# Performance work log

Hardware: AMD Instinct MI355X
Metric: run time of the kernel (lower is better)

The kernel has to match this reference:

```python
import jax, jax.numpy as jnp
import numpy as np

N, E, IN, H, OUT, CD = 50000, 800000, 64, 128, 128, 2


def _lin(key, fi, fo):
    # PyTorch nn.Linear default init: U(-1/sqrt(fan_in), 1/sqrt(fan_in))
    k1, k2 = jax.random.split(key)
    s = 1.0 / np.sqrt(fi)
    W = jax.random.uniform(k1, (fi, fo), minval=-s, maxval=s, dtype=jnp.float32)
    b = jax.random.uniform(k2, (fo,), minval=-s, maxval=s, dtype=jnp.float32)
    return W, b


def setup_inputs() -> dict:
    key = jax.random.key(0)
    ks = jax.random.split(key, 12)
    feat = jax.random.normal(ks[0], (N, IN), dtype=jnp.float32)
    offsets = jax.random.normal(ks[1], (E, CD), dtype=jnp.float32)
    src = jax.random.randint(ks[2], (E,), 0, N)
    dst = jax.random.randint(ks[3], (E,), 0, N)
    kW1, kb1 = _lin(ks[4], CD, H)
    kW2, kb2 = _lin(ks[5], H, IN)
    sW1, sb1 = _lin(ks[6], IN, H)
    sW2, sb2 = _lin(ks[7], H, H)
    mW1, mb1 = _lin(ks[8], IN + H, H)
    mW2, mb2 = _lin(ks[9], H, H)
    mW3, mb3 = _lin(ks[10], H, H)
    mW4, mb4 = _lin(ks[11], H, OUT)
    return dict(feat=feat, offsets=offsets, src=src, dst=dst,
                kW1=kW1, kb1=kb1, kW2=kW2, kb2=kb2,
                sW1=sW1, sb1=sb1, sW2=sW2, sb2=sb2,
                mW1=mW1, mb1=mb1, mW2=mW2, mb2=mb2,
                mW3=mW3, mb3=mb3, mW4=mW4, mb4=mb4)


def reference(feat, offsets, src, dst, kW1, kb1, kW2, kb2, sW1, sb1, sW2, sb2,
              mW1, mb1, mW2, mb2, mW3, mb3, mW4, mb4):
    elu = jax.nn.elu
    n = feat.shape[0]
    # per-edge kernel weights from offsets: [E, IN]
    kw = elu(offsets @ kW1 + kb1) @ kW2 + kb2
    # dist_fn == 'eculidean': score = 1 / (||offsets||_1 + 0.001), edge softmax per dst node
    score = 1.0 / (jnp.sum(jnp.abs(offsets), axis=1) + 0.001)  # [E]
    mx = jax.lax.stop_gradient(jax.ops.segment_max(score, dst, num_segments=n))
    ex = jnp.exp(score - mx[dst])
    w = ex / jax.ops.segment_sum(ex, dst, num_segments=n)[dst]  # [E]
    # u_mul_e + sum aggregation: gather src feats, scale by per-edge weights, scatter-add to dst
    m = feat[src] * (w[:, None] * kw)                     # [E, IN]
    agg = jax.ops.segment_sum(m, dst, num_segments=n)     # [N, IN]
    # self branch
    h_self = elu(feat @ sW1 + sb1) @ sW2 + sb2            # [N, H]
    # concat + MLP head
    h = jnp.concatenate([agg, h_self], axis=1)            # [N, IN+H]
    h = elu(h @ mW1 + mb1)
    h = elu(h @ mW2 + mb2)
    h = elu(h @ mW3 + mb3)
    return h @ mW4 + mb4                                  # [N, OUT]
```

## Files before the change

kernel.cpp:

```cpp
#include <hip/hip_runtime.h>
#include <hip/hip_bf16.h>
#include <math.h>

#define N_NODES 50000
#define N_EDGES 800000
#define NB_SCAN ((N_NODES + 255) / 256)

typedef _Float16 half8 __attribute__((ext_vector_type(8)));
typedef _Float16 half4 __attribute__((ext_vector_type(4)));
typedef float f32x4 __attribute__((ext_vector_type(4)));

__device__ __forceinline__ float elu_f(float x) { return x > 0.f ? x : __expf(x) - 1.f; }
__device__ __forceinline__ float edge_score(float2 o) {
    return 1.f / (fabsf(o.x) + fabsf(o.y) + 0.001f);
}

__global__ __launch_bounds__(256)
void k_deg(const int* __restrict__ dst, int* __restrict__ deg) {
    int e = blockIdx.x * 256 + threadIdx.x;
    if (e >= N_EDGES) return;
    atomicAdd(&deg[dst[e]], 1);
}

__global__ __launch_bounds__(256)
void k_bsum(const int* __restrict__ deg, int* __restrict__ bsum) {
    int i = blockIdx.x * 256 + threadIdx.x;
    int v = (i < N_NODES) ? deg[i] : 0;
    #pragma unroll
    for (int d = 32; d; d >>= 1) v += __shfl_xor(v, d);
    __shared__ int ws[4];
    if ((threadIdx.x & 63) == 0) ws[threadIdx.x >> 6] = v;
    __syncthreads();
    if (threadIdx.x == 0) bsum[blockIdx.x] = ws[0] + ws[1] + ws[2] + ws[3];
}

__global__ __launch_bounds__(256)
void k_bscan(const int* __restrict__ bsum, int* __restrict__ bpre, int* __restrict__ rs) {
    const int t = threadIdx.x, lane = t & 63, wv = t >> 6;
    int v = (t < NB_SCAN) ? bsum[t] : 0;
    int inc = v;
    #pragma unroll
    for (int d = 1; d < 64; d <<= 1) { int u = __shfl_up(inc, d); if (lane >= d) inc += u; }
    __shared__ int wtot[4];
    if (lane == 63) wtot[wv] = inc;
    __syncthreads();
    int add = 0;
    for (int w = 0; w < wv; ++w) add += wtot[w];
    if (t < NB_SCAN) bpre[t] = inc + add - v;
    if (t == 0) rs[N_NODES] = N_EDGES;
}

__global__ __launch_bounds__(256)
void k_wr(const int* __restrict__ deg, const int* __restrict__ bpre,
          int* __restrict__ rs, int* __restrict__ cur) {
    const int i = blockIdx.x * 256 + threadIdx.x;
    const int lane = threadIdx.x & 63, wv = threadIdx.x >> 6;
    int v = (i < N_NODES) ? deg[i] : 0;
    int inc = v;
    #pragma unroll
    for (int d = 1; d < 64; d <<= 1) { int u = __shfl_up(inc, d); if (lane >= d) inc += u; }
    __shared__ int wtot[4];
    if (lane == 63) wtot[wv] = inc;
    __syncthreads();
    int add = bpre[blockIdx.x];
    for (int w = 0; w < wv; ++w) add += wtot[w];
    if (i < N_NODES) { int excl = inc - v + add; rs[i] = excl; cur[i] = excl; }
}

__global__ __launch_bounds__(256)
void k_fill(const int* __restrict__ dst, const int* __restrict__ src,
            const float* __restrict__ off2, int* __restrict__ cur,
            float2* __restrict__ off2c, float* __restrict__ score_csr,
            int* __restrict__ src_csr) {
    int e = blockIdx.x * 256 + threadIdx.x;
    if (e >= N_EDGES) return;
    float2 o = ((const float2*)off2)[e];
    int p = atomicAdd(&cur[dst[e]], 1);
    off2c[p] = o;
    score_csr[p] = edge_score(o);
    src_csr[p] = src[e];
}

#define WTOT 98304
#define KW2TOT 8192
__global__ __launch_bounds__(256)
void k_wsplit(const float* __restrict__ sW1, const float* __restrict__ sW2,
              const float* __restrict__ mW1, const float* __restrict__ mW2,
              const float* __restrict__ mW3, const float* __restrict__ mW4,
              const float* __restrict__ kW2,
              _Float16* __restrict__ wsH, _Float16* __restrict__ wsL,
              _Float16* __restrict__ wkH, _Float16* __restrict__ wkL) {
    int idx = blockIdx.x * 256 + threadIdx.x;
    if (idx < WTOT) {
        const float* W; int base, K;
        if      (idx < 8192)  { W = sW1; base = 0;     K = 64;  }
        else if (idx < 24576) { W = sW2; base = 8192;  K = 128; }
        else if (idx < 49152) { W = mW1; base = 24576; K = 192; }
        else if (idx < 65536) { W = mW2; base = 49152; K = 128; }
        else if (idx < 81920) { W = mW3; base = 65536; K = 128; }
        else                  { W = mW4; base = 81920; K = 128; }
        int local = idx - base;
        int k = local >> 7, col = local & 127;
        int nt = col >> 4, colg = col & 15;
        int kt = k >> 5, lq = (k >> 3) & 3, i = k & 7;
        int fi = base + ((nt * (K >> 5) + kt) * 4 + lq) * 128 + colg * 8 + i;
        float w = W[k * 128 + col];
        _Float16 h = (_Float16)w;
        wsH[fi] = h;
        wsL[fi] = (_Float16)(w - (float)h);
    } else if (idx < WTOT + KW2TOT) {
        int x = idx - WTOT;
        int i = x & 7, colg = (x >> 3) & 15;
        int lq = (x >> 7) & 3, kt = (x >> 9) & 3, jt = x >> 11;
        int k = kt * 32 + lq * 8 + i;
        int j = jt * 16 + colg;
        float w = kW2[k * 64 + j];
        _Float16 h = (_Float16)w;
        wkH[x] = h;
        wkL[x] = (_Float16)(w - (float)h);
    }
}

__global__ __launch_bounds__(256)
void k_kw(const float2* __restrict__ off2c,
          const float* __restrict__ kW1, const float* __restrict__ kb1,
          const _Float16* __restrict__ wkH, const _Float16* __restrict__ wkL,
          const float* __restrict__ kb2, _Float16* __restrict__ kwbuf) {
    const int t = threadIdx.x;
    const int lane = t & 63, wv = t >> 6;
    const int pb = blockIdx.x * 128 + wv * 32;
    const int colg = lane & 15, lq = lane >> 4;

    float2 o[2];
    #pragma unroll
    for (int et = 0; et < 2; ++et)
        o[et] = off2c[pb + et * 16 + colg];

    f32x4 c[2][4];
    #pragma unroll
    for (int et = 0; et < 2; ++et)
        #pragma unroll
        for (int jt = 0; jt < 4; ++jt) c[et][jt] = (f32x4){0.f, 0.f, 0.f, 0.f};

    #pragma unroll
    for (int kt = 0; kt < 4; ++kt) {
        const int k0 = kt * 32 + lq * 8;
        float4 a0 = *(const float4*)&kW1[k0];
        float4 a1 = *(const float4*)&kW1[k0 + 4];
        float4 b0 = *(const float4*)&kW1[128 + k0];
        float4 b1 = *(const float4*)&kW1[128 + k0 + 4];
        float4 c0 = *(const float4*)&kb1[k0];
        float4 c1 = *(const float4*)&kb1[k0 + 4];
        const float wa[8] = {a0.x, a0.y, a0.z, a0.w, a1.x, a1.y, a1.z, a1.w};
        const float wb[8] = {b0.x, b0.y, b0.z, b0.w, b1.x, b1.y, b1.z, b1.w};
        const float bb[8] = {c0.x, c0.y, c0.z, c0.w, c1.x, c1.y, c1.z, c1.w};

        half8 Bh[2], Bl[2];
        #pragma unroll
        for (int et = 0; et < 2; ++et) {
            #pragma unroll
            for (int i = 0; i < 8; ++i) {
                float h = elu_f(fmaf(o[et].y, wb[i], fmaf(o[et].x, wa[i], bb[i])));
                _Float16 hh = (_Float16)h;
                Bh[et][i] = hh;
                Bl[et][i] = (_Float16)(h - (float)hh);
            }
        }
        #pragma unroll
        for (int jt = 0; jt < 4; ++jt) {
            int fo = ((jt * 4 + kt) * 4 + lq) * 128 + colg * 8;
            half8 Ah = *(const half8*)&wkH[fo];
            half8 Al = *(const half8*)&wkL[fo];
            #pragma unroll
            for (int et = 0; et < 2; ++et) {
                c[et][jt] = __builtin_amdgcn_mfma_f32_16x16x32_f16(Ah, Bh[et], c[et][jt], 0, 0, 0);
                c[et][jt] = __builtin_amdgcn_mfma_f32_16x16x32_f16(Ah, Bl[et], c[et][jt], 0, 0, 0);
                c[et][jt] = __builtin_amdgcn_mfma_f32_16x16x32_f16(Al, Bh[et], c[et][jt], 0, 0, 0);
            }
        }
    }

    #pragma unroll
    for (int jt = 0; jt < 4; ++jt) {
        const int j0 = jt * 16 + lq * 4;
        float4 bv = *(const float4*)&kb2[j0];
        const float bias4[4] = {bv.x, bv.y, bv.z, bv.w};
        #pragma unroll
        for (int et = 0; et < 2; ++et) {
            const int p = pb + et * 16 + colg;
            half4 v;
            #pragma unroll
            for (int r = 0; r < 4; ++r) v[r] = (_Float16)(c[et][jt][r] + bias4[r]);
            *(half4*)&kwbuf[(size_t)p * 64 + j0] = v;
        }
    }
}

__global__ __launch_bounds__(256)
void k_agg(const float* __restrict__ score_csr, const int* __restrict__ src_csr,
           const int* __restrict__ rs, const float* __restrict__ feat,
           const _Float16* __restrict__ kwbuf, float* __restrict__ agg) {
    const int lane = threadIdx.x & 63;
    const int wav  = threadIdx.x >> 6;
    const int gw   = blockIdx.x * 4 + wav;
    const int nw   = gridDim.x * 4;

    for (int n = gw; n < N_NODES; n += nw) {
        const int p0 = rs[n], p1 = rs[n + 1];
        if (p0 == p1) { agg[(size_t)n * 64 + lane] = 0.f; continue; }

        float mx = 0.f;
        for (int p = p0 + lane; p < p1; p += 64) mx = fmaxf(mx, score_csr[p]);
        #pragma unroll
        for (int d = 32; d; d >>= 1) mx = fmaxf(mx, __shfl_xor(mx, d));

        float sm = 0.f;
        for (int p = p0 + lane; p < p1; p += 64) sm += __expf(score_csr[p] - mx);
        #pragma unroll
        for (int d = 32; d; d >>= 1) sm += __shfl_xor(sm, d);
        const float dinv = 1.f / sm;

        float a0 = 0.f, a1 = 0.f, a2 = 0.f, a3 = 0.f;
        int p = p0;
        for (; p + 4 <= p1; p += 4) {
            float w0 = __expf(score_csr[p]     - mx) * dinv;
            float w1 = __expf(score_csr[p + 1] - mx) * dinv;
            float w2 = __expf(score_csr[p + 2] - mx) * dinv;
            float w3 = __expf(score_csr[p + 3] - mx) * dinv;
            const int s0 = src_csr[p], s1 = src_csr[p + 1];
            const int s2 = src_csr[p + 2], s3 = src_csr[p + 3];
            float f0 = feat[(size_t)s0 * 64 + lane];
            float f1 = feat[(size_t)s1 * 64 + lane];
            float f2 = feat[(size_t)s2 * 64 + lane];
            float f3 = feat[(size_t)s3 * 64 + lane];
            float k0 = (float)kwbuf[(size_t)(p)     * 64 + lane];
            float k1 = (float)kwbuf[(size_t)(p + 1) * 64 + lane];
            float k2 = (float)kwbuf[(size_t)(p + 2) * 64 + lane];
            float k3 = (float)kwbuf[(size_t)(p + 3) * 64 + lane];
            a0 = fmaf(f0 * w0, k0, a0);
            a1 = fmaf(f1 * w1, k1, a1);
            a2 = fmaf(f2 * w2, k2, a2);
            a3 = fmaf(f3 * w3, k3, a3);
        }
        for (; p < p1; ++p) {
            float wgt = __expf(score_csr[p] - mx) * dinv;
            float f = feat[(size_t)src_csr[p] * 64 + lane];
            float kv = (float)kwbuf[(size_t)p * 64 + lane];
            a0 = fmaf(f * wgt, kv, a0);
        }
        agg[(size_t)n * 64 + lane] = (a0 + a1) + (a2 + a3);
    }
}

__device__ __forceinline__
void mm64(const char* XH, const char* XL, const _Float16* __restrict__ WH,
          const _Float16* __restrict__ WL, int K, int lane, int wv, f32x4 c[4][2]) {
    const int colg = lane & 15, lq = lane >> 4;
    #pragma unroll
    for (int m = 0; m < 4; ++m)
        #pragma unroll
        for (int j = 0; j < 2; ++j) c[m][j] = (f32x4){0.f, 0.f, 0.f, 0.f};
    const int KT = K >> 5;
    for (int kt = 0; kt < KT; ++kt) {
        half8 Bh[2], Bl[2], Ah[4], Al[4];
        #pragma unroll
        for (int j = 0; j < 2; ++j) {
            int fo = ((((wv * 2 + j) * KT + kt) * 4 + lq) * 128) + colg * 8;
            Bh[j] = *(const half8*)&WH[fo];
            Bl[j] = *(const half8*)&WL[fo];
        }
        #pragma unroll
        for (int m = 0; m < 4; ++m) {
            int row = m * 16 + colg;
            int byte = ((row * K + kt * 32 + lq * 8) * 2) ^ ((row & 7) << 4);
            Ah[m] = *(const half8*)(XH + byte);
            Al[m] = *(const half8*)(XL + byte);
        }
        #pragma unroll
        for (int m = 0; m < 4; ++m)
            #pragma unroll
            for (int j = 0; j < 2; ++j) {
                c[m][j] = __builtin_amdgcn_mfma_f32_16x16x32_f16(Ah[m], Bh[j], c[m][j], 0, 0, 0);
                c[m][j] = __builtin_amdgcn_mfma_f32_16x16x32_f16(Ah[m], Bl[j], c[m][j], 0, 0, 0);
                c[m][j] = __builtin_amdgcn_mfma_f32_16x16x32_f16(Al[m], Bh[j], c[m][j], 0, 0, 0);
            }
    }
}

__device__ __forceinline__
void mm64_h1(const half8 aggH[4][2], const half8 aggL[4][2],
             const char* XH, const char* XL,
             const _Float16* __restrict__ WH, const _Float16* __restrict__ WL,
             int lane, int wv, f32x4 c[4][2]) {
    const int colg = lane & 15, lq = lane >> 4;
    #pragma unroll
    for (int m = 0; m < 4; ++m)
        #pragma unroll
        for (int j = 0; j < 2; ++j) c[m][j] = (f32x4){0.f, 0.f, 0.f, 0.f};
    #pragma unroll
    for (int kt = 0; kt < 6; ++kt) {
        half8 Bh[2], Bl[2], Ah[4], Al[4];
        #pragma unroll
        for (int j = 0; j < 2; ++j) {
            int fo = ((((wv * 2 + j) * 6 + kt) * 4 + lq) * 128) + colg * 8;
            Bh[j] = *(const half8*)&WH[fo];
            Bl[j] = *(const half8*)&WL[fo];
        }
        if (kt < 2) {
            #pragma unroll
            for (int m = 0; m < 4; ++m) { Ah[m] = aggH[m][kt]; Al[m] = aggL[m][kt]; }
        } else {
            #pragma unroll
            for (int m = 0; m < 4; ++m) {
                int row = m * 16 + colg;
                int byte = ((row * 128 + (kt - 2) * 32 + lq * 8) * 2) ^ ((row & 7) << 4);
                Ah[m] = *(const half8*)(XH + byte);
                Al[m] = *(const half8*)(XL + byte);
            }
        }
        #pragma unroll
        for (int m = 0; m < 4; ++m)
            #pragma unroll
            for (int j = 0; j < 2; ++j) {
                c[m][j] = __builtin_amdgcn_mfma_f32_16x16x32_f16(Ah[m], Bh[j], c[m][j], 0, 0, 0);
                c[m][j] = __builtin_amdgcn_mfma_f32_16x16x32_f16(Ah[m], Bl[j], c[m][j], 0, 0, 0);
                c[m][j] = __builtin_amdgcn_mfma_f32_16x16x32_f16(Al[m], Bh[j], c[m][j], 0, 0, 0);
            }
    }
}

__device__ __forceinline__
void epi_lds(char* XH, char* XL, int lane, int wv,
             f32x4 c[4][2], const float* __restrict__ bias, bool do_elu) {
    const int colg = lane & 15, lq = lane >> 4;
    float bj[2] = { bias[wv * 32 + colg], bias[wv * 32 + 16 + colg] };
    #pragma unroll
    for (int m = 0; m < 4; ++m)
        #pragma unroll
        for (int j = 0; j < 2; ++j) {
            int col = wv * 32 + j * 16 + colg;
            #pragma unroll
            for (int r = 0; r < 4; ++r) {
                int row = m * 16 + lq * 4 + r;
                float v = c[m][j][r] + bj[j];
                if (do_elu) v = elu_f(v);
                _Float16 h = (_Float16)v;
                int byte = ((row * 128 + col) * 2) ^ ((row & 7) << 4);
                *(_Float16*)(XH + byte) = h;
                *(_Float16*)(XL + byte) = (_Float16)(v - (float)h);
            }
        }
}

__global__ __launch_bounds__(256)
void k_node(const float* __restrict__ feat, const float* __restrict__ agg,
            const _Float16* __restrict__ wsH, const _Float16* __restrict__ wsL,
            const float* __restrict__ sb1, const float* __restrict__ sb2,
            const float* __restrict__ mb1, const float* __restrict__ mb2,
            const float* __restrict__ mb3, const float* __restrict__ mb4,
            float* __restrict__ out) {
    __shared__ _Float16 XH[64 * 128];
    __shared__ _Float16 XL[64 * 128];
    const int t = threadIdx.x;
    const int lane = t & 63, wv = t >> 6;
    const int colg = lane & 15, lq = lane >> 4;
    const int row0 = blockIdx.x * 64;
    f32x4 c[4][2];

    {
        int r = t >> 2, c4 = (t & 3) * 4;
        #pragma unroll
        for (int q = 0; q < 4; ++q) {
            int col = (c4 + q) * 4;
            float4 v = make_float4(0.f, 0.f, 0.f, 0.f);
            if (row0 + r < N_NODES) v = *(const float4*)&feat[(size_t)(row0 + r) * 64 + col];
            _Float16 h4h[4], h4l[4];
            float vv[4] = {v.x, v.y, v.z, v.w};
            #pragma unroll
            for (int i = 0; i < 4; ++i) {
                _Float16 h = (_Float16)vv[i];
                h4h[i] = h; h4l[i] = (_Float16)(vv[i] - (float)h);
            }
            int byte = ((r * 64 + col) * 2) ^ ((r & 7) << 4);
            *(ulong1*)((char*)XH + byte) = *(ulong1*)h4h;
            *(ulong1*)((char*)XL + byte) = *(ulong1*)h4l;
        }
    }
    __syncthreads();

    mm64((const char*)XH, (const char*)XL, wsH + 0, wsL + 0, 64, lane, wv, c);
    __syncthreads();
    epi_lds((char*)XH, (char*)XL, lane, wv, c, sb1, true);
    __syncthreads();

    mm64((const char*)XH, (const char*)XL, wsH + 8192, wsL + 8192, 128, lane, wv, c);

    half8 aggH[4][2], aggL[4][2];
    #pragma unroll
    for (int m = 0; m < 4; ++m) {
        int row = row0 + m * 16 + colg;
        #pragma unroll
        for (int kt = 0; kt < 2; ++kt) {
            int k0 = kt * 32 + lq * 8;
            float4 v0 = make_float4(0.f, 0.f, 0.f, 0.f), v1 = v0;
            if (row < N_NODES) {
                v0 = *(const float4*)&agg[(size_t)row * 64 + k0];
                v1 = *(const float4*)&agg[(size_t)row * 64 + k0 + 4];
            }
            float vv[8] = {v0.x, v0.y, v0.z, v0.w, v1.x, v1.y, v1.z, v1.w};
            #pragma unroll
            for (int i = 0; i < 8; ++i) {
                _Float16 h = (_Float16)vv[i];
                aggH[m][kt][i] = h;
                aggL[m][kt][i] = (_Float16)(vv[i] - (float)h);
            }
        }
    }
    __syncthreads();
    epi_lds((char*)XH, (char*)XL, lane, wv, c, sb2, false);
    __syncthreads();

    mm64_h1(aggH, aggL, (const char*)XH, (const char*)XL,
            wsH + 24576, wsL + 24576, lane, wv, c);
    __syncthreads();
    epi_lds((char*)XH, (char*)XL, lane, wv, c, mb1, true);
    __syncthreads();

    mm64((const char*)XH, (const char*)XL, wsH + 49152, wsL + 49152, 128, lane, wv, c);
    __syncthreads();
    epi_lds((char*)XH, (char*)XL, lane, wv, c, mb2, true);
    __syncthreads();

    mm64((const char*)XH, (const char*)XL, wsH + 65536, wsL + 65536, 128, lane, wv, c);
    __syncthreads();
    epi_lds((char*)XH, (char*)XL, lane, wv, c, mb3, true);
    __syncthreads();

    mm64((const char*)XH, (const char*)XL, wsH + 81920, wsL + 81920, 128, lane, wv, c);
    {
        float bj[2] = { mb4[wv * 32 + colg], mb4[wv * 32 + 16 + colg] };
        #pragma unroll
        for (int m = 0; m < 4; ++m)
            #pragma unroll
            for (int j = 0; j < 2; ++j) {
                int col = wv * 32 + j * 16 + colg;
                #pragma unroll
                for (int r = 0; r < 4; ++r) {
                    int row = row0 + m * 16 + lq * 4 + r;
                    if (row < N_NODES)
                        out[(size_t)row * 128 + col] = c[m][j][r] + bj[j];
                }
            }
    }
}

extern "C" void kernel_launch(void* const* d_in, const int* in_sizes, int n_in,
                              void* d_out, int out_size, void* d_ws, size_t ws_size,
                              hipStream_t stream) {
    (void)in_sizes; (void)n_in; (void)out_size; (void)ws_size;
    const float* feat = (const float*)d_in[0];
    const float* off2 = (const float*)d_in[1];
    const int*   src  = (const int*)d_in[2];
    const int*   dst  = (const int*)d_in[3];
    const float* kW1  = (const float*)d_in[4];
    const float* kb1  = (const float*)d_in[5];
    const float* kW2  = (const float*)d_in[6];
    const float* kb2  = (const float*)d_in[7];
    const float* sW1  = (const float*)d_in[8];
    const float* sb1  = (const float*)d_in[9];
    const float* sW2  = (const float*)d_in[10];
    const float* sb2  = (const float*)d_in[11];
    const float* mW1  = (const float*)d_in[12];
    const float* mb1  = (const float*)d_in[13];
    const float* mW2  = (const float*)d_in[14];
    const float* mb2  = (const float*)d_in[15];
    const float* mW3  = (const float*)d_in[16];
    const float* mb3  = (const float*)d_in[17];
    const float* mW4  = (const float*)d_in[18];
    const float* mb4  = (const float*)d_in[19];

    char* ws = (char*)d_ws;
    size_t off = 0;
    auto alloc = [&](size_t bytes) -> void* {
        void* p = ws + off;
        off += (bytes + 255) & ~(size_t)255;
        return p;
    };
    int*    deg    = (int*)alloc((size_t)N_NODES * 4);
    int*    rs     = (int*)alloc((size_t)(N_NODES + 8) * 4);
    int*    cur    = (int*)alloc((size_t)N_NODES * 4);
    int*    bsum   = (int*)alloc((size_t)NB_SCAN * 4);
    int*    bpre   = (int*)alloc((size_t)NB_SCAN * 4);
    float2* off2c  = (float2*)alloc((size_t)N_EDGES * 8);
    float*  scorec = (float*)alloc((size_t)N_EDGES * 4);
    int*    srcc   = (int*)alloc((size_t)N_EDGES * 4);
    float*  agg    = (float*)alloc((size_t)N_NODES * 64 * 4);
    _Float16* wsH  = (_Float16*)alloc((size_t)WTOT * 2);
    _Float16* wsL  = (_Float16*)alloc((size_t)WTOT * 2);
    _Float16* wkH  = (_Float16*)alloc((size_t)KW2TOT * 2);
    _Float16* wkL  = (_Float16*)alloc((size_t)KW2TOT * 2);
    _Float16* kwbuf = (_Float16*)alloc((size_t)N_EDGES * 64 * 2);

    hipMemsetAsync(deg, 0, (size_t)N_NODES * 4, stream);

    const int EB = (N_EDGES + 255) / 256;
    const int GB = (N_NODES + 63) / 64;

    k_deg   <<<EB, 256, 0, stream>>>(dst, deg);
    k_bsum  <<<NB_SCAN, 256, 0, stream>>>(deg, bsum);
    k_bscan <<<1, 256, 0, stream>>>(bsum, bpre, rs);
    k_wr    <<<NB_SCAN, 256, 0, stream>>>(deg, bpre, rs, cur);
    k_fill  <<<EB, 256, 0, stream>>>(dst, src, off2, cur, off2c, scorec, srcc);
    k_wsplit<<<(WTOT + KW2TOT + 255) / 256, 256, 0, stream>>>(sW1, sW2, mW1, mW2, mW3, mW4,
                                                              kW2, wsH, wsL, wkH, wkL);

    k_kw <<<N_EDGES / 128, 256, 0, stream>>>(off2c, kW1, kb1, wkH, wkL, kb2, kwbuf);
    k_agg<<<2048, 256, 0, stream>>>(scorec, srcc, rs, feat, kwbuf, agg);

    k_node<<<GB, 256, 0, stream>>>(feat, agg, wsH, wsL, sb1, sb2, mb1, mb2, mb3, mb4,
                                   (float*)d_out);
}
```

Baseline: 283.1 us.

## Fuse per-edge kernel-weight MLP with aggregation via shared-memory tile

The per-edge kernel-weight computation is merged into the aggregation kernel. Each block computes the kw values for 128 consecutive CSR edges into LDS, then aggregates them into their destination nodes. Softmax max and normalizer are computed up front by a separate per-node kernel. This removes the round trip of the 800000x64 half-precision kwbuf through global memory. In exchange it adds a binary search per block, float atomics for nodes whose edges span block boundaries, and an extra memset of agg. Per-block load may also become less balanced.

```diff
diff --git a/kernel.cpp b/kernel.cpp
--- a/kernel.cpp
+++ b/kernel.cpp
@@ -122,84 +122,8 @@
 }
 
 __global__ __launch_bounds__(256)
-void k_kw(const float2* __restrict__ off2c,
-          const float* __restrict__ kW1, const float* __restrict__ kb1,
-          const _Float16* __restrict__ wkH, const _Float16* __restrict__ wkL,
-          const float* __restrict__ kb2, _Float16* __restrict__ kwbuf) {
-    const int t = threadIdx.x;
-    const int lane = t & 63, wv = t >> 6;
-    const int pb = blockIdx.x * 128 + wv * 32;
-    const int colg = lane & 15, lq = lane >> 4;
-
-    float2 o[2];
-    #pragma unroll
-    for (int et = 0; et < 2; ++et)
-        o[et] = off2c[pb + et * 16 + colg];
-
-    f32x4 c[2][4];
-    #pragma unroll
-    for (int et = 0; et < 2; ++et)
-        #pragma unroll
-        for (int jt = 0; jt < 4; ++jt) c[et][jt] = (f32x4){0.f, 0.f, 0.f, 0.f};
-
-    #pragma unroll
-    for (int kt = 0; kt < 4; ++kt) {
-        const int k0 = kt * 32 + lq * 8;
-        float4 a0 = *(const float4*)&kW1[k0];
-        float4 a1 = *(const float4*)&kW1[k0 + 4];
-        float4 b0 = *(const float4*)&kW1[128 + k0];
-        float4 b1 = *(const float4*)&kW1[128 + k0 + 4];
-        float4 c0 = *(const float4*)&kb1[k0];
-        float4 c1 = *(const float4*)&kb1[k0 + 4];
-        const float wa[8] = {a0.x, a0.y, a0.z, a0.w, a1.x, a1.y, a1.z, a1.w};
-        const float wb[8] = {b0.x, b0.y, b0.z, b0.w, b1.x, b1.y, b1.z, b1.w};
-        const float bb[8] = {c0.x, c0.y, c0.z, c0.w, c1.x, c1.y, c1.z, c1.w};
-
-        half8 Bh[2], Bl[2];
-        #pragma unroll
-        for (int et = 0; et < 2; ++et) {
-            #pragma unroll
-            for (int i = 0; i < 8; ++i) {
-                float h = elu_f(fmaf(o[et].y, wb[i], fmaf(o[et].x, wa[i], bb[i])));
-                _Float16 hh = (_Float16)h;
-                Bh[et][i] = hh;
-                Bl[et][i] = (_Float16)(h - (float)hh);
-            }
-        }
-        #pragma unroll
-        for (int jt = 0; jt < 4; ++jt) {
-            int fo = ((jt * 4 + kt) * 4 + lq) * 128 + colg * 8;
-            half8 Ah = *(const half8*)&wkH[fo];
-            half8 Al = *(const half8*)&wkL[fo];
-            #pragma unroll
-            for (int et = 0; et < 2; ++et) {
-                c[et][jt] = __builtin_amdgcn_mfma_f32_16x16x32_f16(Ah, Bh[et], c[et][jt], 0, 0, 0);
-                c[et][jt] = __builtin_amdgcn_mfma_f32_16x16x32_f16(Ah, Bl[et], c[et][jt], 0, 0, 0);
-                c[et][jt] = __builtin_amdgcn_mfma_f32_16x16x32_f16(Al, Bh[et], c[et][jt], 0, 0, 0);
-            }
-        }
-    }
-
-    #pragma unroll
-    for (int jt = 0; jt < 4; ++jt) {
-        const int j0 = jt * 16 + lq * 4;
-        float4 bv = *(const float4*)&kb2[j0];
-        const float bias4[4] = {bv.x, bv.y, bv.z, bv.w};
-        #pragma unroll
-        for (int et = 0; et < 2; ++et) {
-            const int p = pb + et * 16 + colg;
-            half4 v;
-            #pragma unroll
-            for (int r = 0; r < 4; ++r) v[r] = (_Float16)(c[et][jt][r] + bias4[r]);
-            *(half4*)&kwbuf[(size_t)p * 64 + j0] = v;
-        }
-    }
-}
-
-__global__ __launch_bounds__(256)
-void k_agg(const float* __restrict__ score_csr, const int* __restrict__ src_csr,
-           const int* __restrict__ rs, const float* __restrict__ feat,
-           const _Float16* __restrict__ kwbuf, float* __restrict__ agg) {
+void k_soft(const float* __restrict__ score_csr, const int* __restrict__ rs,
+            float* __restrict__ mx, float* __restrict__ dinv) {
     const int lane = threadIdx.x & 63;
     const int wav  = threadIdx.x >> 6;
     const int gw   = blockIdx.x * 4 + wav;
@@ -207,48 +131,135 @@
 
     for (int n = gw; n < N_NODES; n += nw) {
         const int p0 = rs[n], p1 = rs[n + 1];
-        if (p0 == p1) { agg[(size_t)n * 64 + lane] = 0.f; continue; }
-
-        float mx = 0.f;
-        for (int p = p0 + lane; p < p1; p += 64) mx = fmaxf(mx, score_csr[p]);
-        #pragma unroll
-        for (int d = 32; d; d >>= 1) mx = fmaxf(mx, __shfl_xor(mx, d));
-
+        if (p0 == p1) { if (lane == 0) { mx[n] = 0.f; dinv[n] = 0.f; } continue; }
+        float m = 0.f;
+        for (int p = p0 + lane; p < p1; p += 64) m = fmaxf(m, score_csr[p]);
+        #pragma unroll
+        for (int d = 32; d; d >>= 1) m = fmaxf(m, __shfl_xor(m, d));
         float sm = 0.f;
-        for (int p = p0 + lane; p < p1; p += 64) sm += __expf(score_csr[p] - mx);
+        for (int p = p0 + lane; p < p1; p += 64) sm += __expf(score_csr[p] - m);
         #pragma unroll
         for (int d = 32; d; d >>= 1) sm += __shfl_xor(sm, d);
-        const float dinv = 1.f / sm;
-
-        float a0 = 0.f, a1 = 0.f, a2 = 0.f, a3 = 0.f;
-        int p = p0;
-        for (; p + 4 <= p1; p += 4) {
-            float w0 = __expf(score_csr[p]     - mx) * dinv;
-            float w1 = __expf(score_csr[p + 1] - mx) * dinv;
-            float w2 = __expf(score_csr[p + 2] - mx) * dinv;
-            float w3 = __expf(score_csr[p + 3] - mx) * dinv;
-            const int s0 = src_csr[p], s1 = src_csr[p + 1];
-            const int s2 = src_csr[p + 2], s3 = src_csr[p + 3];
-            float f0 = feat[(size_t)s0 * 64 + lane];
-            float f1 = feat[(size_t)s1 * 64 + lane];
-            float f2 = feat[(size_t)s2 * 64 + lane];
-            float f3 = feat[(size_t)s3 * 64 + lane];
-            float k0 = (float)kwbuf[(size_t)(p)     * 64 + lane];
-            float k1 = (float)kwbuf[(size_t)(p + 1) * 64 + lane];
-            float k2 = (float)kwbuf[(size_t)(p + 2) * 64 + lane];
-            float k3 = (float)kwbuf[(size_t)(p + 3) * 64 + lane];
-            a0 = fmaf(f0 * w0, k0, a0);
-            a1 = fmaf(f1 * w1, k1, a1);
-            a2 = fmaf(f2 * w2, k2, a2);
-            a3 = fmaf(f3 * w3, k3, a3);
-        }
-        for (; p < p1; ++p) {
-            float wgt = __expf(score_csr[p] - mx) * dinv;
-            float f = feat[(size_t)src_csr[p] * 64 + lane];
-            float kv = (float)kwbuf[(size_t)p * 64 + lane];
-            a0 = fmaf(f * wgt, kv, a0);
-        }
-        agg[(size_t)n * 64 + lane] = (a0 + a1) + (a2 + a3);
+        if (lane == 0) { mx[n] = m; dinv[n] = 1.f / sm; }
+    }
+}
+
+#define KWPAD 68
+__global__ __launch_bounds__(256)
+void k_edge(const float2* __restrict__ off2c, const float* __restrict__ score_csr,
+            const int* __restrict__ src_csr, const int* __restrict__ rs,
+            const float* __restrict__ feat,
+            const float* __restrict__ kW1, const float* __restrict__ kb1,
+            const _Float16* __restrict__ wkH, const _Float16* __restrict__ wkL,
+            const float* __restrict__ kb2,
+            const float* __restrict__ mx, const float* __restrict__ dinv,
+            float* __restrict__ agg) {
+    __shared__ _Float16 kwl[128 * KWPAD];
+    const int t = threadIdx.x;
+    const int lane = t & 63, wv = t >> 6;
+    const int pb  = blockIdx.x * 128;
+    const int wpb = pb + wv * 32;
+    const int colg = lane & 15, lq = lane >> 4;
+
+    {
+        float2 o[2];
+        #pragma unroll
+        for (int et = 0; et < 2; ++et)
+            o[et] = off2c[wpb + et * 16 + colg];
+
+        f32x4 c[2][4];
+        #pragma unroll
+        for (int et = 0; et < 2; ++et)
+            #pragma unroll
+            for (int jt = 0; jt < 4; ++jt) c[et][jt] = (f32x4){0.f, 0.f, 0.f, 0.f};
+
+        #pragma unroll
+        for (int kt = 0; kt < 4; ++kt) {
+            const int k0 = kt * 32 + lq * 8;
+            float4 a0 = *(const float4*)&kW1[k0];
+            float4 a1 = *(const float4*)&kW1[k0 + 4];
+            float4 b0 = *(const float4*)&kW1[128 + k0];
+            float4 b1 = *(const float4*)&kW1[128 + k0 + 4];
+            float4 c0 = *(const float4*)&kb1[k0];
+            float4 c1 = *(const float4*)&kb1[k0 + 4];
+            const float wa[8] = {a0.x, a0.y, a0.z, a0.w, a1.x, a1.y, a1.z, a1.w};
+            const float wb[8] = {b0.x, b0.y, b0.z, b0.w, b1.x, b1.y, b1.z, b1.w};
+            const float bb[8] = {c0.x, c0.y, c0.z, c0.w, c1.x, c1.y, c1.z, c1.w};
+
+            half8 Bh[2], Bl[2];
+            #pragma unroll
+            for (int et = 0; et < 2; ++et) {
+                #pragma unroll
+                for (int i = 0; i < 8; ++i) {
+                    float h = elu_f(fmaf(o[et].y, wb[i], fmaf(o[et].x, wa[i], bb[i])));
+                    _Float16 hh = (_Float16)h;
+                    Bh[et][i] = hh;
+                    Bl[et][i] = (_Float16)(h - (float)hh);
+                }
+            }
+            #pragma unroll
+            for (int jt = 0; jt < 4; ++jt) {
+                int fo = ((jt * 4 + kt) * 4 + lq) * 128 + colg * 8;
+                half8 Ah = *(const half8*)&wkH[fo];
+                half8 Al = *(const half8*)&wkL[fo];
+                #pragma unroll
+                for (int et = 0; et < 2; ++et) {
+                    c[et][jt] = __builtin_amdgcn_mfma_f32_16x16x32_f16(Ah, Bh[et], c[et][jt], 0, 0, 0);
+                    c[et][jt] = __builtin_amdgcn_mfma_f32_16x16x32_f16(Ah, Bl[et], c[et][jt], 0, 0, 0);
+                    c[et][jt] = __builtin_amdgcn_mfma_f32_16x16x32_f16(Al, Bh[et], c[et][jt], 0, 0, 0);
+                }
+            }
+        }
+
+        #pragma unroll
+        for (int jt = 0; jt < 4; ++jt) {
+            const int j0 = jt * 16 + lq * 4;
+            float4 bv = *(const float4*)&kb2[j0];
+            const float bias4[4] = {bv.x, bv.y, bv.z, bv.w};
+            #pragma unroll
+            for (int et = 0; et < 2; ++et) {
+                const int ls = wv * 32 + et * 16 + colg;
+                half4 v;
+                #pragma unroll
+                for (int r = 0; r < 4; ++r) v[r] = (_Float16)(c[et][jt][r] + bias4[r]);
+                *(half4*)&kwl[ls * KWPAD + j0] = v;
+            }
+        }
+    }
+    __syncthreads();
+
+    int lo = 0, hi = N_NODES - 1;
+    while (lo < hi) { int mid = (lo + hi) >> 1; if (rs[mid + 1] > pb) hi = mid; else lo = mid + 1; }
+    const int pe = pb + 128;
+
+    for (int n = lo + wv; n < N_NODES && rs[n] < pe; n += 4) {
+        const int s0 = rs[n], s1 = rs[n + 1];
+        const int a = s0 > pb ? s0 : pb;
+        const int b = s1 < pe ? s1 : pe;
+        if (a >= b) continue;
+        const bool full = (s0 >= pb) && (s1 <= pe);
+        const float mxn = mx[n], dvn = dinv[n];
+        float acc0 = 0.f, acc1 = 0.f;
+        int s = a;
+        for (; s + 2 <= b; s += 2) {
+            float w0 = __expf(score_csr[s]     - mxn) * dvn;
+            float w1 = __expf(score_csr[s + 1] - mxn) * dvn;
+            float f0 = feat[(size_t)src_csr[s]     * 64 + lane];
+            float f1 = feat[(size_t)src_csr[s + 1] * 64 + lane];
+            float k0 = (float)kwl[(s - pb)     * KWPAD + lane];
+            float k1 = (float)kwl[(s + 1 - pb) * KWPAD + lane];
+            acc0 = fmaf(f0 * w0, k0, acc0);
+            acc1 = fmaf(f1 * w1, k1, acc1);
+        }
+        if (s < b) {
+            float w0 = __expf(score_csr[s] - mxn) * dvn;
+            float f0 = feat[(size_t)src_csr[s] * 64 + lane];
+            float k0 = (float)kwl[(s - pb) * KWPAD + lane];
+            acc0 = fmaf(f0 * w0, k0, acc0);
+        }
+        float acc = acc0 + acc1;
+        if (full) agg[(size_t)n * 64 + lane] = acc;
+        else      atomicAdd(&agg[(size_t)n * 64 + lane], acc);
     }
 }
 
@@ -494,14 +505,16 @@
     float2* off2c  = (float2*)alloc((size_t)N_EDGES * 8);
     float*  scorec = (float*)alloc((size_t)N_EDGES * 4);
     int*    srcc   = (int*)alloc((size_t)N_EDGES * 4);
+    float*  smx    = (float*)alloc((size_t)N_NODES * 4);
+    float*  sdinv  = (float*)alloc((size_t)N_NODES * 4);
     float*  agg    = (float*)alloc((size_t)N_NODES * 64 * 4);
     _Float16* wsH  = (_Float16*)alloc((size_t)WTOT * 2);
     _Float16* wsL  = (_Float16*)alloc((size_t)WTOT * 2);
     _Float16* wkH  = (_Float16*)alloc((size_t)KW2TOT * 2);
     _Float16* wkL  = (_Float16*)alloc((size_t)KW2TOT * 2);
-    _Float16* kwbuf = (_Float16*)alloc((size_t)N_EDGES * 64 * 2);
 
     hipMemsetAsync(deg, 0, (size_t)N_NODES * 4, stream);
+    hipMemsetAsync(agg, 0, (size_t)N_NODES * 64 * 4, stream);
 
     const int EB = (N_EDGES + 255) / 256;
     const int GB = (N_NODES + 63) / 64;
@@ -513,9 +526,11 @@
     k_fill  <<<EB, 256, 0, stream>>>(dst, src, off2, cur, off2c, scorec, srcc);
     k_wsplit<<<(WTOT + KW2TOT + 255) / 256, 256, 0, stream>>>(sW1, sW2, mW1, mW2, mW3, mW4,
                                                               kW2, wsH, wsL, wkH, wkL);
-
-    k_kw <<<N_EDGES / 128, 256, 0, stream>>>(off2c, kW1, kb1, wkH, wkL, kb2, kwbuf);
-    k_agg<<<2048, 256, 0, stream>>>(scorec, srcc, rs, feat, kwbuf, agg);
+    k_soft  <<<2048, 256, 0, stream>>>(scorec, rs, smx, sdinv);
+
+    k_edge<<<N_EDGES / 128, 256, 0, stream>>>(off2c, scorec, srcc, rs, feat,
+                                              kW1, kb1, wkH, wkL, kb2,
+                                              smx, sdinv, agg);
 
     k_node<<<GB, 256, 0, stream>>>(feat, agg, wsH, wsL, sb1, sb2, mb1, mb2, mb3, mb4,
                                    (float*)d_out);
```

Result: slower. 328.5 us (+16.0%).

## Restructure node MLP kernel to one wave per 32-row tile, removing block barriers

Applied to the files above, without the earlier changes.

The node MLP kernel now runs one 64-thread wave per block. Each block owns 32 rows and computes all 128 output columns, where before four waves each computed a 32-column slice of 64 rows. Every __syncthreads is replaced by a wave-local LDS wait fence, since only one wave touches the shared tile. The cost is that each wave now streams the full weight matrices, so per-row global and L2 weight traffic is higher. Each lane also holds 16 accumulator vectors, which raises register pressure.

```diff
diff --git a/kernel.cpp b/kernel.cpp
--- a/kernel.cpp
+++ b/kernel.cpp
@@ -252,66 +252,63 @@
     }
 }
 
+__device__ __forceinline__ void wave_lds_fence() {
+    asm volatile("s_waitcnt lgkmcnt(0)" ::: "memory");
+    __builtin_amdgcn_sched_barrier(0);
+}
+
 __device__ __forceinline__
-void mm64(const char* XH, const char* XL, const _Float16* __restrict__ WH,
-          const _Float16* __restrict__ WL, int K, int lane, int wv, f32x4 c[4][2]) {
+void mmrow(const char* XH, const char* XL, const _Float16* __restrict__ WH,
+           const _Float16* __restrict__ WL, int K, int lane, f32x4 c[2][8]) {
     const int colg = lane & 15, lq = lane >> 4;
     #pragma unroll
-    for (int m = 0; m < 4; ++m)
-        #pragma unroll
-        for (int j = 0; j < 2; ++j) c[m][j] = (f32x4){0.f, 0.f, 0.f, 0.f};
+    for (int m = 0; m < 2; ++m)
+        #pragma unroll
+        for (int jt = 0; jt < 8; ++jt) c[m][jt] = (f32x4){0.f, 0.f, 0.f, 0.f};
     const int KT = K >> 5;
     for (int kt = 0; kt < KT; ++kt) {
-        half8 Bh[2], Bl[2], Ah[4], Al[4];
-        #pragma unroll
-        for (int j = 0; j < 2; ++j) {
-            int fo = ((((wv * 2 + j) * KT + kt) * 4 + lq) * 128) + colg * 8;
-            Bh[j] = *(const half8*)&WH[fo];
-            Bl[j] = *(const half8*)&WL[fo];
-        }
-        #pragma unroll
-        for (int m = 0; m < 4; ++m) {
+        half8 Ah[2], Al[2];
+        #pragma unroll
+        for (int m = 0; m < 2; ++m) {
             int row = m * 16 + colg;
             int byte = ((row * K + kt * 32 + lq * 8) * 2) ^ ((row & 7) << 4);
             Ah[m] = *(const half8*)(XH + byte);
             Al[m] = *(const half8*)(XL + byte);
         }
         #pragma unroll
-        for (int m = 0; m < 4; ++m)
-            #pragma unroll
-            for (int j = 0; j < 2; ++j) {
-                c[m][j] = __builtin_amdgcn_mfma_f32_16x16x32_f16(Ah[m], Bh[j], c[m][j], 0, 0, 0);
-                c[m][j] = __builtin_amdgcn_mfma_f32_16x16x32_f16(Ah[m], Bl[j], c[m][j], 0, 0, 0);
-                c[m][j] = __builtin_amdgcn_mfma_f32_16x16x32_f16(Al[m], Bh[j], c[m][j], 0, 0, 0);
-            }
+        for (int jt = 0; jt < 8; ++jt) {
+            int fo = ((jt * KT + kt) * 4 + lq) * 128 + colg * 8;
+            half8 Bh = *(const half8*)&WH[fo];
+            half8 Bl = *(const half8*)&WL[fo];
+            #pragma unroll
+            for (int m = 0; m < 2; ++m) {
+                c[m][jt] = __builtin_amdgcn_mfma_f32_16x16x32_f16(Ah[m], Bh, c[m][jt], 0, 0, 0);
+                c[m][jt] = __builtin_amdgcn_mfma_f32_16x16x32_f16(Ah[m], Bl, c[m][jt], 0, 0, 0);
+                c[m][jt] = __builtin_amdgcn_mfma_f32_16x16x32_f16(Al[m], Bh, c[m][jt], 0, 0, 0);
+            }
+        }
     }
 }
 
 __device__ __forceinline__
-void mm64_h1(const half8 aggH[4][2], const half8 aggL[4][2],
-             const char* XH, const char* XL,
-             const _Float16* __restrict__ WH, const _Float16* __restrict__ WL,
-             int lane, int wv, f32x4 c[4][2]) {
+void mmrow_h1(const half8 agH[2][2], const half8 agL[2][2],
+              const char* XH, const char* XL,
+              const _Float16* __restrict__ WH, const _Float16* __restrict__ WL,
+              int lane, f32x4 c[2][8]) {
     const int colg = lane & 15, lq = lane >> 4;
     #pragma unroll
-    for (int m = 0; m < 4; ++m)
-        #pragma unroll
-        for (int j = 0; j < 2; ++j) c[m][j] = (f32x4){0.f, 0.f, 0.f, 0.f};
+    for (int m = 0; m < 2; ++m)
+        #pragma unroll
+        for (int jt = 0; jt < 8; ++jt) c[m][jt] = (f32x4){0.f, 0.f, 0.f, 0.f};
     #pragma unroll
     for (int kt = 0; kt < 6; ++kt) {
-        half8 Bh[2], Bl[2], Ah[4], Al[4];
-        #pragma unroll
-        for (int j = 0; j < 2; ++j) {
-            int fo = ((((wv * 2 + j) * 6 + kt) * 4 + lq) * 128) + colg * 8;
-            Bh[j] = *(const half8*)&WH[fo];
-            Bl[j] = *(const half8*)&WL[fo];
-        }
+        half8 Ah[2], Al[2];
         if (kt < 2) {
             #pragma unroll
-            for (int m = 0; m < 4; ++m) { Ah[m] = aggH[m][kt]; Al[m] = aggL[m][kt]; }
+            for (int m = 0; m < 2; ++m) { Ah[m] = agH[m][kt]; Al[m] = agL[m][kt]; }
         } else {
             #pragma unroll
-            for (int m = 0; m < 4; ++m) {
+            for (int m = 0; m < 2; ++m) {
                 int row = m * 16 + colg;
                 int byte = ((row * 128 + (kt - 2) * 32 + lq * 8) * 2) ^ ((row & 7) << 4);
                 Ah[m] = *(const half8*)(XH + byte);
@@ -319,85 +316,85 @@
             }
         }
         #pragma unroll
-        for (int m = 0; m < 4; ++m)
-            #pragma unroll
-            for (int j = 0; j < 2; ++j) {
-                c[m][j] = __builtin_amdgcn_mfma_f32_16x16x32_f16(Ah[m], Bh[j], c[m][j], 0, 0, 0);
-                c[m][j] = __builtin_amdgcn_mfma_f32_16x16x32_f16(Ah[m], Bl[j], c[m][j], 0, 0, 0);
-                c[m][j] = __builtin_amdgcn_mfma_f32_16x16x32_f16(Al[m], Bh[j], c[m][j], 0, 0, 0);
-            }
+        for (int jt = 0; jt < 8; ++jt) {
+            int fo = ((jt * 6 + kt) * 4 + lq) * 128 + colg * 8;
+            half8 Bh = *(const half8*)&WH[fo];
+            half8 Bl = *(const half8*)&WL[fo];
+            #pragma unroll
+            for (int m = 0; m < 2; ++m) {
+                c[m][jt] = __builtin_amdgcn_mfma_f32_16x16x32_f16(Ah[m], Bh, c[m][jt], 0, 0, 0);
+                c[m][jt] = __builtin_amdgcn_mfma_f32_16x16x32_f16(Ah[m], Bl, c[m][jt], 0, 0, 0);
+                c[m][jt] = __builtin_amdgcn_mfma_f32_16x16x32_f16(Al[m], Bh, c[m][jt], 0, 0, 0);
+            }
+        }
     }
 }
 
 __device__ __forceinline__
-void epi_lds(char* XH, char* XL, int lane, int wv,
-             f32x4 c[4][2], const float* __restrict__ bias, bool do_elu) {
+void epirow(char* XH, char* XL, int lane, f32x4 c[2][8],
+            const float* __restrict__ bias, bool do_elu) {
     const int colg = lane & 15, lq = lane >> 4;
-    float bj[2] = { bias[wv * 32 + colg], bias[wv * 32 + 16 + colg] };
-    #pragma unroll
-    for (int m = 0; m < 4; ++m)
-        #pragma unroll
-        for (int j = 0; j < 2; ++j) {
-            int col = wv * 32 + j * 16 + colg;
+    #pragma unroll
+    for (int jt = 0; jt < 8; ++jt) {
+        float bj = bias[jt * 16 + colg];
+        #pragma unroll
+        for (int m = 0; m < 2; ++m) {
             #pragma unroll
             for (int r = 0; r < 4; ++r) {
                 int row = m * 16 + lq * 4 + r;
-                float v = c[m][j][r] + bj[j];
+                float v = c[m][jt][r] + bj;
                 if (do_elu) v = elu_f(v);
                 _Float16 h = (_Float16)v;
-                int byte = ((row * 128 + col) * 2) ^ ((row & 7) << 4);
+                int byte = ((row * 128 + jt * 16 + colg) * 2) ^ ((row & 7) << 4);
                 *(_Float16*)(XH + byte) = h;
                 *(_Float16*)(XL + byte) = (_Float16)(v - (float)h);
             }
         }
-}
-
-__global__ __launch_bounds__(256)
+    }
+    wave_lds_fence();
+}
+
+__global__ __launch_bounds__(64)
 void k_node(const float* __restrict__ feat, const float* __restrict__ agg,
             const _Float16* __restrict__ wsH, const _Float16* __restrict__ wsL,
             const float* __restrict__ sb1, const float* __restrict__ sb2,
             const float* __restrict__ mb1, const float* __restrict__ mb2,
             const float* __restrict__ mb3, const float* __restrict__ mb4,
             float* __restrict__ out) {
-    __shared__ _Float16 XH[64 * 128];
-    __shared__ _Float16 XL[64 * 128];
-    const int t = threadIdx.x;
-    const int lane = t & 63, wv = t >> 6;
+    __shared__ _Float16 XH[32 * 128];
+    __shared__ _Float16 XL[32 * 128];
+    const int lane = threadIdx.x;
     const int colg = lane & 15, lq = lane >> 4;
-    const int row0 = blockIdx.x * 64;
-    f32x4 c[4][2];
-
-    {
-        int r = t >> 2, c4 = (t & 3) * 4;
-        #pragma unroll
-        for (int q = 0; q < 4; ++q) {
-            int col = (c4 + q) * 4;
-            float4 v = make_float4(0.f, 0.f, 0.f, 0.f);
-            if (row0 + r < N_NODES) v = *(const float4*)&feat[(size_t)(row0 + r) * 64 + col];
-            _Float16 h4h[4], h4l[4];
-            float vv[4] = {v.x, v.y, v.z, v.w};
-            #pragma unroll
-            for (int i = 0; i < 4; ++i) {
-                _Float16 h = (_Float16)vv[i];
-                h4h[i] = h; h4l[i] = (_Float16)(vv[i] - (float)h);
-            }
-            int byte = ((r * 64 + col) * 2) ^ ((r & 7) << 4);
-            *(ulong1*)((char*)XH + byte) = *(ulong1*)h4h;
-            *(ulong1*)((char*)XL + byte) = *(ulong1*)h4l;
-        }
-    }
-    __syncthreads();
-
-    mm64((const char*)XH, (const char*)XL, wsH + 0, wsL + 0, 64, lane, wv, c);
-    __syncthreads();
-    epi_lds((char*)XH, (char*)XL, lane, wv, c, sb1, true);
-    __syncthreads();
-
-    mm64((const char*)XH, (const char*)XL, wsH + 8192, wsL + 8192, 128, lane, wv, c);
-
-    half8 aggH[4][2], aggL[4][2];
-    #pragma unroll
-    for (int m = 0; m < 4; ++m) {
+    const int row0 = blockIdx.x * 32;
+    f32x4 c[2][8];
+
+    #pragma unroll
+    for (int q = 0; q < 8; ++q) {
+        int idx = q * 64 + lane;
+        int r = idx >> 4, c4 = idx & 15;
+        float4 v = make_float4(0.f, 0.f, 0.f, 0.f);
+        if (row0 + r < N_NODES) v = *(const float4*)&feat[(size_t)(row0 + r) * 64 + c4 * 4];
+        _Float16 h4h[4], h4l[4];
+        float vv[4] = {v.x, v.y, v.z, v.w};
+        #pragma unroll
+        for (int i = 0; i < 4; ++i) {
+            _Float16 h = (_Float16)vv[i];
+            h4h[i] = h; h4l[i] = (_Float16)(vv[i] - (float)h);
+        }
+        int byte = ((r * 64 + c4 * 4) * 2) ^ ((r & 7) << 4);
+        *(ulong1*)((char*)XH + byte) = *(ulong1*)h4h;
+        *(ulong1*)((char*)XL + byte) = *(ulong1*)h4l;
+    }
+    wave_lds_fence();
+
+    mmrow((const char*)XH, (const char*)XL, wsH + 0, wsL + 0, 64, lane, c);
+    epirow((char*)XH, (char*)XL, lane, c, sb1, true);
+
+    mmrow((const char*)XH, (const char*)XL, wsH + 8192, wsL + 8192, 128, lane, c);
+
+    half8 agH[2][2], agL[2][2];
+    #pragma unroll
+    for (int m = 0; m < 2; ++m) {
         int row = row0 + m * 16 + colg;
         #pragma unroll
         for (int kt = 0; kt < 2; ++kt) {
@@ -411,46 +408,36 @@
             #pragma unroll
             for (int i = 0; i < 8; ++i) {
                 _Float16 h = (_Float16)vv[i];
-                aggH[m][kt][i] = h;
-                aggL[m][kt][i] = (_Float16)(vv[i] - (float)h);
-            }
-        }
-    }
-    __syncthreads();
-    epi_lds((char*)XH, (char*)XL, lane, wv, c, sb2, false);
-    __syncthreads();
-
-    mm64_h1(aggH, aggL, (const char*)XH, (const char*)XL,
-            wsH + 24576, wsL + 24576, lane, wv, c);
-    __syncthreads();
-    epi_lds((char*)XH, (char*)XL, lane, wv, c, mb1, true);
-    __syncthreads();
-
-    mm64((const char*)XH, (const char*)XL, wsH + 49152, wsL + 49152, 128, lane, wv, c);
-    __syncthreads();
-    epi_lds((char*)XH, (char*)XL, lane, wv, c, mb2, true);
-    __syncthreads();
-
-    mm64((const char*)XH, (const char*)XL, wsH + 65536, wsL + 65536, 128, lane, wv, c);
-    __syncthreads();
-    epi_lds((char*)XH, (char*)XL, lane, wv, c, mb3, true);
-    __syncthreads();
-
-    mm64((const char*)XH, (const char*)XL, wsH + 81920, wsL + 81920, 128, lane, wv, c);
-    {
-        float bj[2] = { mb4[wv * 32 + colg], mb4[wv * 32 + 16 + colg] };
-        #pragma unroll
-        for (int m = 0; m < 4; ++m)
-            #pragma unroll
-            for (int j = 0; j < 2; ++j) {
-                int col = wv * 32 + j * 16 + colg;
-                #pragma unroll
-                for (int r = 0; r < 4; ++r) {
-                    int row = row0 + m * 16 + lq * 4 + r;
-                    if (row < N_NODES)
-                        out[(size_t)row * 128 + col] = c[m][j][r] + bj[j];
-                }
-            }
+                agH[m][kt][i] = h;
+                agL[m][kt][i] = (_Float16)(vv[i] - (float)h);
+            }
+        }
+    }
+    epirow((char*)XH, (char*)XL, lane, c, sb2, false);
+
+    mmrow_h1(agH, agL, (const char*)XH, (const char*)XL,
+             wsH + 24576, wsL + 24576, lane, c);
+    epirow((char*)XH, (char*)XL, lane, c, mb1, true);
+
+    mmrow((const char*)XH, (const char*)XL, wsH + 49152, wsL + 49152, 128, lane, c);
+    epirow((char*)XH, (char*)XL, lane, c, mb2, true);
+
+    mmrow((const char*)XH, (const char*)XL, wsH + 65536, wsL + 65536, 128, lane, c);
+    epirow((char*)XH, (char*)XL, lane, c, mb3, true);
+
+    mmrow((const char*)XH, (const char*)XL, wsH + 81920, wsL + 81920, 128, lane, c);
+    #pragma unroll
+    for (int jt = 0; jt < 8; ++jt) {
+        float bj = mb4[jt * 16 + colg];
+        #pragma unroll
+        for (int m = 0; m < 2; ++m) {
+            #pragma unroll
+            for (int r = 0; r < 4; ++r) {
+                int row = row0 + m * 16 + lq * 4 + r;
+                if (row < N_NODES)
+                    out[(size_t)row * 128 + jt * 16 + colg] = c[m][jt][r] + bj;
+            }
+        }
     }
 }
 
@@ -504,7 +491,7 @@
     hipMemsetAsync(deg, 0, (size_t)N_NODES * 4, stream);
 
     const int EB = (N_EDGES + 255) / 256;
-    const int GB = (N_NODES + 63) / 64;
+    const int NBNODE = (N_NODES + 31) / 32;
 
     k_deg   <<<EB, 256, 0, stream>>>(dst, deg);
     k_bsum  <<<NB_SCAN, 256, 0, stream>>>(deg, bsum);
@@ -517,6 +504,6 @@
     k_kw <<<N_EDGES / 128, 256, 0, stream>>>(off2c, kW1, kb1, wkH, wkL, kb2, kwbuf);
     k_agg<<<2048, 256, 0, stream>>>(scorec, srcc, rs, feat, kwbuf, agg);
 
-    k_node<<<GB, 256, 0, stream>>>(feat, agg, wsH, wsL, sb1, sb2, mb1, mb2, mb3, mb4,
-                                   (float*)d_out);
-}
+    k_node<<<NBNODE, 64, 0, stream>>>(feat, agg, wsH, wsL, sb1, sb2, mb1, mb2, mb3, mb4,
+                                      (float*)d_out);
+}
```

Result: slower. 352.2 us (+24.4%).
